# Optimization experiments

Hardware: AMD Instinct MI355X
Metric: run time of the kernel (lower is better)

Reference implementation:

```python
import jax, jax.numpy as jnp
import numpy as np

VOCAB = 1_000_000
EMBED = 128
BATCH = 16384
N_POS = 10   # window_size * 2
N_NEG = 50   # window_size * 2 * K


def setup_inputs() -> dict:
    key = jax.random.key(0)
    k1, k2, k3, k4, k5 = jax.random.split(key, 5)
    return {
        "input_labels": jax.random.randint(k1, (BATCH, 1), 0, VOCAB),
        "pos_labels": jax.random.randint(k2, (BATCH, N_POS), 0, VOCAB),
        "neg_labels": jax.random.randint(k3, (BATCH, N_NEG), 0, VOCAB),
        "in_embed": jax.random.normal(k4, (VOCAB, EMBED), dtype=jnp.float32),
        "out_embed": jax.random.normal(k5, (VOCAB, EMBED), dtype=jnp.float32),
    }


def reference(input_labels, pos_labels, neg_labels, in_embed, out_embed):
    # center word embedding: [B, E] (input_labels is [B, 1])
    v = in_embed[input_labels[:, 0]]
    pos = out_embed[pos_labels]          # [B, P, E]
    neg = out_embed[neg_labels]          # [B, N, E]
    pos_dot = jnp.einsum("bpe,be->bp", pos, v)   # bmm(pos, v[:, :, None]).squeeze(2)
    neg_dot = -jnp.einsum("bne,be->bn", neg, v)  # bmm(neg, -v[:, :, None]).squeeze(2)
    log_pos = jax.nn.log_sigmoid(pos_dot).sum(axis=1)
    log_neg = jax.nn.log_sigmoid(neg_dot).sum(axis=1)
    return -(log_pos + log_neg)          # [B]
```

## Files before the change

kernel.cpp:

```cpp
#include <hip/hip_runtime.h>
#include <math.h>

#define EMBED 128
#define NPOS  10
#define NNEG  50

__device__ __forceinline__ float logsigmoid(float x) {
    return fminf(x, 0.0f) - log1pf(__expf(-fabsf(x)));
}

__device__ __forceinline__ float waveReduceSum(float x) {
    #pragma unroll
    for (int off = 32; off > 0; off >>= 1)
        x += __shfl_xor(x, off, 64);
    return x;
}

__global__ __launch_bounds__(256) void nsloss_kernel(
    const int*   __restrict__ input_labels,
    const int*   __restrict__ pos_labels,
    const int*   __restrict__ neg_labels,
    const float* __restrict__ in_embed,
    const float* __restrict__ out_embed,
    float*       __restrict__ out,
    int batch)
{
    const int wave = (int)((blockIdx.x * blockDim.x + threadIdx.x) >> 6);
    const int lane = (int)(threadIdx.x & 63);
    if (wave >= batch) return;
    const int b = wave;

    const long vrow = (long)input_labels[b] * EMBED;
    const float2 v = *reinterpret_cast<const float2*>(in_embed + vrow + 2 * lane);

    float loss = 0.0f;

    const int* __restrict__ pl = pos_labels + (long)b * NPOS;
    #pragma unroll
    for (int s = 0; s < NPOS; ++s) {
        const long rrow = (long)pl[s] * EMBED;
        const float2 r = *reinterpret_cast<const float2*>(out_embed + rrow + 2 * lane);
        float p = v.x * r.x + v.y * r.y;
        const float dot = waveReduceSum(p);
        loss += logsigmoid(dot);
    }

    const int* __restrict__ nl = neg_labels + (long)b * NNEG;
    #pragma unroll 10
    for (int s = 0; s < NNEG; ++s) {
        const long rrow = (long)nl[s] * EMBED;
        const float2 r = *reinterpret_cast<const float2*>(out_embed + rrow + 2 * lane);
        float p = v.x * r.x + v.y * r.y;
        const float dot = waveReduceSum(p);
        loss += logsigmoid(-dot);
    }

    if (lane == 0) out[b] = -loss;
}

extern "C" void kernel_launch(void* const* d_in, const int* in_sizes, int n_in,
                              void* d_out, int out_size, void* d_ws, size_t ws_size,
                              hipStream_t stream) {
    const int*   input_labels = (const int*)d_in[0];
    const int*   pos_labels   = (const int*)d_in[1];
    const int*   neg_labels   = (const int*)d_in[2];
    const float* in_embed     = (const float*)d_in[3];
    const float* out_embed    = (const float*)d_in[4];
    float*       out          = (float*)d_out;

    const int batch = in_sizes[0];
    const int wavesPerBlock = 4;
    const int blocks = (batch + wavesPerBlock - 1) / wavesPerBlock;

    nsloss_kernel<<<blocks, wavesPerBlock * 64, 0, stream>>>(
        input_labels, pos_labels, neg_labels, in_embed, out_embed, out, batch);
}
```

Baseline: 908.9 us.

## Process four embedding rows per wave pass with 16-lane groups

Each wave now splits into four 16-lane groups, and each group dot-products a different context row using two float4 loads per lane. The old scheme used the whole wave per row with float2 loads. Labels are loaded once, one per lane, and broadcast with shuffles, which replaces repeated scalar label reads. The cross-lane reduction per row shrinks from six shuffle steps to four, and there are fifteen passes instead of sixty. This aims to cut reduction and latency overhead and put more independent gathers in flight. The trade-off is more register use per lane for the float4 loads.

Result: faster. 830.7 us (-8.6%).

```diff
diff --git a/kernel.cpp b/kernel.cpp
--- a/kernel.cpp
+++ b/kernel.cpp
@@ -4,16 +4,11 @@
 #define EMBED 128
 #define NPOS  10
 #define NNEG  50
+#define NTOT  (NPOS + NNEG)
+#define NPASS (NTOT / 4)
 
 __device__ __forceinline__ float logsigmoid(float x) {
     return fminf(x, 0.0f) - log1pf(__expf(-fabsf(x)));
-}
-
-__device__ __forceinline__ float waveReduceSum(float x) {
-    #pragma unroll
-    for (int off = 32; off > 0; off >>= 1)
-        x += __shfl_xor(x, off, 64);
-    return x;
 }
 
 __global__ __launch_bounds__(256) void nsloss_kernel(
@@ -25,35 +20,45 @@
     float*       __restrict__ out,
     int batch)
 {
-    const int wave = (int)((blockIdx.x * blockDim.x + threadIdx.x) >> 6);
+    const int wid  = (int)((blockIdx.x * blockDim.x + threadIdx.x) >> 6);
     const int lane = (int)(threadIdx.x & 63);
-    if (wave >= batch) return;
-    const int b = wave;
+    if (wid >= batch) return;
+    const int b = wid;
+    const int g = lane >> 4;
+    const int e = lane & 15;
 
     const long vrow = (long)input_labels[b] * EMBED;
-    const float2 v = *reinterpret_cast<const float2*>(in_embed + vrow + 2 * lane);
+    const float4 v0 = *reinterpret_cast<const float4*>(in_embed + vrow + 8 * e);
+    const float4 v1 = *reinterpret_cast<const float4*>(in_embed + vrow + 8 * e + 4);
+
+    int myLabel = 0;
+    if (lane < NPOS)      myLabel = pos_labels[(long)b * NPOS + lane];
+    else if (lane < NTOT) myLabel = neg_labels[(long)b * NNEG + (lane - NPOS)];
 
     float loss = 0.0f;
 
-    const int* __restrict__ pl = pos_labels + (long)b * NPOS;
-    #pragma unroll
-    for (int s = 0; s < NPOS; ++s) {
-        const long rrow = (long)pl[s] * EMBED;
-        const float2 r = *reinterpret_cast<const float2*>(out_embed + rrow + 2 * lane);
-        float p = v.x * r.x + v.y * r.y;
-        const float dot = waveReduceSum(p);
-        loss += logsigmoid(dot);
+    #pragma unroll 5
+    for (int p = 0; p < NPASS; ++p) {
+        const int s   = 4 * p + g;
+        const int lbl = __shfl(myLabel, s, 64);
+
+        const float* __restrict__ r = out_embed + (long)lbl * EMBED + 8 * e;
+        const float4 r0 = *reinterpret_cast<const float4*>(r);
+        const float4 r1 = *reinterpret_cast<const float4*>(r + 4);
+
+        float d = v0.x * r0.x + v0.y * r0.y + v0.z * r0.z + v0.w * r0.w
+                + v1.x * r1.x + v1.y * r1.y + v1.z * r1.z + v1.w * r1.w;
+
+        d += __shfl_xor(d, 1, 64);
+        d += __shfl_xor(d, 2, 64);
+        d += __shfl_xor(d, 4, 64);
+        d += __shfl_xor(d, 8, 64);
+
+        loss += logsigmoid((s < NPOS) ? d : -d);
     }
 
-    const int* __restrict__ nl = neg_labels + (long)b * NNEG;
-    #pragma unroll 10
-    for (int s = 0; s < NNEG; ++s) {
-        const long rrow = (long)nl[s] * EMBED;
-        const float2 r = *reinterpret_cast<const float2*>(out_embed + rrow + 2 * lane);
-        float p = v.x * r.x + v.y * r.y;
-        const float dot = waveReduceSum(p);
-        loss += logsigmoid(-dot);
-    }
+    loss += __shfl_xor(loss, 16, 64);
+    loss += __shfl_xor(loss, 32, 64);
 
     if (lane == 0) out[b] = -loss;
 }
```
